# Kernel optimization log

Measured on AMD Instinct MI355X. Metric: run time of the kernel, lower is better.

## Reference

```python
import jax, jax.numpy as jnp
import numpy as np

EPS = 0.0  # GINConv eps

def _gin_conv(x, edge_index, W1, b1, W2, b2, n_nodes):
    # GINConv: mlp((1+eps)*x + sum_{j in N(i)} x_j)
    src, dst = edge_index[0], edge_index[1]
    agg = jax.ops.segment_sum(x[src], dst, num_segments=n_nodes)  # [N, d]
    h = (1.0 + EPS) * x + agg
    h = jax.nn.relu(h @ W1 + b1)  # Linear -> Identity(BN off) -> ReLU
    return h @ W2 + b2            # second Linear


def setup_inputs() -> dict:
    key = jax.random.key(0)
    ks = jax.random.split(key, 10)
    N, E = 50000, 600000
    d_in, d_hid, d_out = 128, 256, 128
    x = jax.random.normal(ks[0], (N, d_in), dtype=jnp.float32)
    edge_index = jax.random.randint(ks[1], (2, E), 0, N, dtype=jnp.int64)

    def lin(k, fan_in, fan_out):
        bound = 1.0 / np.sqrt(fan_in)
        kw, kb = jax.random.split(k)
        W = jax.random.uniform(kw, (fan_in, fan_out), jnp.float32, -bound, bound)
        b = jax.random.uniform(kb, (fan_out,), jnp.float32, -bound, bound)
        return W, b

    W1a, b1a = lin(ks[2], d_in, d_hid)   # conv0 mlp: 128->256
    W2a, b2a = lin(ks[3], d_hid, d_hid)  # conv0 mlp: 256->256
    W1b, b1b = lin(ks[4], d_hid, d_hid)  # conv1 mlp: 256->256
    W2b, b2b = lin(ks[5], d_hid, d_out)  # conv1 mlp: 256->128
    return {"x": x, "W1a": W1a, "b1a": b1a, "W2a": W2a, "b2a": b2a,
            "W1b": W1b, "b1b": b1b, "W2b": W2b, "b2b": b2b,
            "edge_index": edge_index}


def reference(x, W1a, b1a, W2a, b2a, W1b, b1b, W2b, b2b, edge_index):
    n_nodes = x.shape[0]
    # layer 0: GINConv -> relu (use_bn=False; dropout is identity in eval)
    h = _gin_conv(x, edge_index, W1a, b1a, W2a, b2a, n_nodes)
    h = jax.nn.relu(h)
    # final GINConv (no activation after, per forward())
    return _gin_conv(h, edge_index, W1b, b1b, W2b, b2b, n_nodes)
```

## Files before the change

### kernel.cpp

```cpp
#include <hip/hip_runtime.h>


typedef __bf16 bf16x8 __attribute__((ext_vector_type(8)));
typedef float f32x4 __attribute__((ext_vector_type(4)));
typedef float f32x2 __attribute__((ext_vector_type(2)));
typedef unsigned short u16x4 __attribute__((ext_vector_type(4)));
typedef unsigned short u16x8 __attribute__((ext_vector_type(8)));
typedef unsigned int uint32;
typedef uint32 u32x4 __attribute__((ext_vector_type(4)));

#define MAXDEG 48

__device__ __forceinline__ unsigned short f2bf(float f) {
  uint32 u = __builtin_bit_cast(uint32, f);
  u += 0x7FFFu + ((u >> 16) & 1u);
  return (unsigned short)(u >> 16);
}
__device__ __forceinline__ f32x2 bfpair(uint32 w) {
  f32x2 r;
  r.x = __builtin_bit_cast(float, w << 16);
  r.y = __builtin_bit_cast(float, w & 0xFFFF0000u);
  return r;
}

#define G2L16(gp, lp)                                                        \
  __builtin_amdgcn_global_load_lds(                                          \
      (const __attribute__((address_space(1))) void*)(gp),                   \
      (__attribute__((address_space(3))) void*)(lp), 16, 0, 0)

#define BARRIER()                                                            \
  do {                                                                       \
    asm volatile("" ::: "memory");                                           \
    __builtin_amdgcn_s_barrier();                                            \
    asm volatile("" ::: "memory");                                           \
  } while (0)
#define VMCNT0() asm volatile("s_waitcnt vmcnt(0)" ::: "memory")

__global__ __launch_bounds__(256) void prep_fill(
    const int* __restrict__ eidx, int* __restrict__ deg, int* __restrict__ ell,
    int E, int FB,
    const float* __restrict__ x, unsigned short* __restrict__ xb, long long n4,
    const float* __restrict__ W1a, const float* __restrict__ W2a,
    const float* __restrict__ W1b, const float* __restrict__ W2b,
    unsigned short* __restrict__ w1t, unsigned short* __restrict__ w2t,
    unsigned short* __restrict__ w3t, unsigned short* __restrict__ w4t) {
  int b = blockIdx.x;
  int t = threadIdx.x;
  if (b < FB) {
    int e = b * 256 + t;
    if (e < E) {
      int s = eidx[e];
      int d = eidx[e + E];
      int c = atomicAdd(&deg[d], 1);
      if (c < MAXDEG) ell[d * MAXDEG + c] = s;
    }
  } else if (b < FB + 768) {
    int i = (b - FB) * 256 + t;
    const float* W;
    unsigned short* WT;
    int K, N, j;
    if (i < 32768) {
      W = W1a; WT = w1t; K = 128; N = 256; j = i;
    } else if (i < 98304) {
      W = W2a; WT = w2t; K = 256; N = 256; j = i - 32768;
    } else if (i < 163840) {
      W = W1b; WT = w3t; K = 256; N = 256; j = i - 98304;
    } else {
      W = W2b; WT = w4t; K = 256; N = 128; j = i - 163840;
    }
    int k = j / N, n = j - k * N;
    WT[n * K + k] = f2bf(W[j]);
  } else {
    long long i = (long long)(b - FB - 768) * 256 + t;
    long long stride = (long long)(gridDim.x - FB - 768) * 256;
    for (; i < n4; i += stride) {
      float4 v = ((const float4*)x)[i];
      u16x4 o;
      o.x = f2bf(v.x); o.y = f2bf(v.y); o.z = f2bf(v.z); o.w = f2bf(v.w);
      ((u16x4*)xb)[i] = o;
    }
  }
}

template <int K1, int N2, bool OUT_BF16>
__global__ __launch_bounds__(512) void fused_layer(
    const unsigned short* __restrict__ src,
    const int* __restrict__ degv, const int* __restrict__ ell,
    const unsigned short* __restrict__ BT1, const float* __restrict__ b1,
    const unsigned short* __restrict__ BT2, const float* __restrict__ b2,
    void* __restrict__ Cout, int Nn) {
  constexpr int GRP = K1 / 8;
  __shared__ unsigned short Ash[64 * 264];
  __shared__ unsigned short Bs[2][256 * 32];
  const int tid = threadIdx.x;
  const int wave = tid >> 6, lane = tid & 63;
  const int quad = lane >> 4, l16 = lane & 15;
  const int rowBase = blockIdx.x * 64;

#define STAGE1B(buf, kk)                                                     \
  for (int c = tid; c < 1024; c += 512)                                      \
    G2L16(BT1 + (long long)(c >> 2) * K1 + (kk) + (c & 3) * 8,               \
          Bs[buf] + c * 8);
#define STAGE2B(buf, kk)                                                     \
  for (int c = tid; c < N2 * 4; c += 512)                                    \
    G2L16(BT2 + (long long)(c >> 2) * 256 + (kk) + (c & 3) * 8,              \
          Bs[buf] + c * 8);

  STAGE1B(0, 0);

  {
    constexpr int NPG = 64 * GRP / 512;
    const int gid = tid / GRP, gl = tid % GRP;
    const unsigned short* sp = src + gl * 8;
#pragma unroll
    for (int nn = 0; nn < NPG; ++nn) {
      const int lrow = gid * NPG + nn;
      int node = rowBase + lrow;
      if (node > Nn - 1) node = Nn - 1;
      const int beg = node * MAXDEG;
      int deg = degv[node];
      if (deg > MAXDEG) deg = MAXDEG;
      f32x2 acc[4];
      {
        u32x4 w = *(const u32x4*)(sp + (size_t)node * K1);
#pragma unroll
        for (int k = 0; k < 4; ++k) acc[k] = bfpair(w[k]);
      }
      int j = 0;
      for (; j + 8 <= deg; j += 8) {
        int idx[8];
#pragma unroll
        for (int u = 0; u < 8; ++u) idx[u] = ell[beg + j + u];
#pragma unroll
        for (int u = 0; u < 8; ++u) {
          u32x4 w = *(const u32x4*)(sp + (size_t)idx[u] * K1);
#pragma unroll
          for (int k = 0; k < 4; ++k) acc[k] += bfpair(w[k]);
        }
      }
      if (j < deg) {
#pragma unroll
        for (int u = 0; u < 8; ++u) {
          int jj = j + u;
          int e = beg + (jj < deg ? jj : deg - 1);
          float sel = (jj < deg) ? 1.f : 0.f;
          f32x2 fs = {sel, sel};
          int rv = ell[e];
          u32x4 w = *(const u32x4*)(sp + (size_t)rv * K1);
#pragma unroll
          for (int k = 0; k < 4; ++k) acc[k] += bfpair(w[k]) * fs;
        }
      }
      u16x8 o;
#pragma unroll
      for (int k = 0; k < 4; ++k) {
        o[2 * k] = f2bf(acc[k].x);
        o[2 * k + 1] = f2bf(acc[k].y);
      }
      *(u16x8*)(Ash + lrow * 264 + gl * 8) = o;
    }
  }
  __syncthreads();

  constexpr int nk1 = K1 / 32;
  f32x4 acc1[4][2] = {};
  int cur = 0;
  for (int t = 0; t < nk1; ++t) {
    if (t + 1 < nk1) STAGE1B(cur ^ 1, (t + 1) * 32);
    bf16x8 af[4], bfr[2];
#pragma unroll
    for (int mi = 0; mi < 4; ++mi)
      af[mi] = *(const bf16x8*)(Ash + (mi * 16 + l16) * 264 + t * 32 + quad * 8);
#pragma unroll
    for (int ni = 0; ni < 2; ++ni)
      bfr[ni] = *(const bf16x8*)(Bs[cur] + (wave * 32 + ni * 16 + l16) * 32 + quad * 8);
#pragma unroll
    for (int mi = 0; mi < 4; ++mi)
#pragma unroll
      for (int ni = 0; ni < 2; ++ni)
        acc1[mi][ni] = __builtin_amdgcn_mfma_f32_16x16x32_bf16(
            af[mi], bfr[ni], acc1[mi][ni], 0, 0, 0);
    VMCNT0();
    BARRIER();
    cur ^= 1;
  }

  STAGE2B(0, 0);
#pragma unroll
  for (int ni = 0; ni < 2; ++ni) {
    int col = wave * 32 + ni * 16 + l16;
    float bv = b1[col];
#pragma unroll
    for (int mi = 0; mi < 4; ++mi)
#pragma unroll
      for (int r = 0; r < 4; ++r) {
        int row = mi * 16 + quad * 4 + r;
        Ash[row * 264 + col] = f2bf(fmaxf(acc1[mi][ni][r] + bv, 0.f));
      }
  }
  __syncthreads();

  constexpr int NW2 = N2 / 8;
  constexpr int NI2 = NW2 / 16;
  f32x4 acc2[4][NI2] = {};
  cur = 0;
  for (int t = 0; t < 8; ++t) {
    int k2 = t * 32;
    if (t + 1 < 8) STAGE2B(cur ^ 1, k2 + 32);
    bf16x8 af[4], bfr[NI2];
#pragma unroll
    for (int mi = 0; mi < 4; ++mi)
      af[mi] = *(const bf16x8*)(Ash + (mi * 16 + l16) * 264 + k2 + quad * 8);
#pragma unroll
    for (int ni = 0; ni < NI2; ++ni)
      bfr[ni] = *(const bf16x8*)(Bs[cur] + (wave * NW2 + ni * 16 + l16) * 32 + quad * 8);
#pragma unroll
    for (int mi = 0; mi < 4; ++mi)
#pragma unroll
      for (int ni = 0; ni < NI2; ++ni)
        acc2[mi][ni] = __builtin_amdgcn_mfma_f32_16x16x32_bf16(
            af[mi], bfr[ni], acc2[mi][ni], 0, 0, 0);
    VMCNT0();
    BARRIER();
    cur ^= 1;
  }
#pragma unroll
  for (int ni = 0; ni < NI2; ++ni) {
    int col = wave * NW2 + ni * 16 + l16;
    float bv = b2[col];
#pragma unroll
    for (int mi = 0; mi < 4; ++mi)
#pragma unroll
      for (int r = 0; r < 4; ++r) {
        int row = rowBase + mi * 16 + quad * 4 + r;
        if (row < Nn) {
          float o = acc2[mi][ni][r] + bv;
          if (OUT_BF16)
            ((unsigned short*)Cout)[(long long)row * N2 + col] = f2bf(fmaxf(o, 0.f));
          else
            ((float*)Cout)[(long long)row * N2 + col] = o;
        }
      }
  }
#undef STAGE1B
#undef STAGE2B
}

extern "C" void kernel_launch(void* const* d_in, const int* in_sizes, int n_in,
                              void* d_out, int out_size, void* d_ws, size_t ws_size,
                              hipStream_t stream) {
  const float* x   = (const float*)d_in[0];
  const float* W1a = (const float*)d_in[1];
  const float* b1a = (const float*)d_in[2];
  const float* W2a = (const float*)d_in[3];
  const float* b2a = (const float*)d_in[4];
  const float* W1b = (const float*)d_in[5];
  const float* b1b = (const float*)d_in[6];
  const float* W2b = (const float*)d_in[7];
  const float* b2b = (const float*)d_in[8];
  const int*   ei  = (const int*)d_in[9];

  const int Nn = in_sizes[0] / 128;
  const int E  = in_sizes[9] / 2;
  float* out = (float*)d_out;

  unsigned short* h   = (unsigned short*)d_ws;
  unsigned short* xb  = h  + (size_t)Nn * 256;
  unsigned short* w1t = xb + (size_t)Nn * 128;
  unsigned short* w2t = w1t + 256 * 128;
  unsigned short* w3t = w2t + 256 * 256;
  unsigned short* w4t = w3t + 256 * 256;
  int* deg  = (int*)(w4t + 128 * 256);
  int* ell  = deg + Nn;

  dim3 blk(256);
  const int FB = (E + 255) / 256;

  hipMemsetAsync(deg, 0, (size_t)Nn * sizeof(int), stream);
  prep_fill<<<FB + 768 + 2048, blk, 0, stream>>>(
      ei, deg, ell, E, FB, x, xb, (long long)Nn * 128 / 4,
      W1a, W2a, W1b, W2b, w1t, w2t, w3t, w4t);

  int lb = (Nn + 63) / 64;

  fused_layer<128, 256, true><<<lb, dim3(512), 0, stream>>>(
      xb, deg, ell, w1t, b1a, w2t, b2a, h, Nn);
  fused_layer<256, 128, false><<<lb, dim3(512), 0, stream>>>(
      h, deg, ell, w3t, b1b, w4t, b2b, out, Nn);
}
```

Baseline: 250.7 us.

## Replace double-buffered weight staging with single LDS buffer and syncthreads

```diff
diff --git a/kernel.cpp b/kernel.cpp
--- a/kernel.cpp
+++ b/kernel.cpp
@@ -27,14 +27,6 @@
   __builtin_amdgcn_global_load_lds(                                          \
       (const __attribute__((address_space(1))) void*)(gp),                   \
       (__attribute__((address_space(3))) void*)(lp), 16, 0, 0)
-
-#define BARRIER()                                                            \
-  do {                                                                       \
-    asm volatile("" ::: "memory");                                           \
-    __builtin_amdgcn_s_barrier();                                            \
-    asm volatile("" ::: "memory");                                           \
-  } while (0)
-#define VMCNT0() asm volatile("s_waitcnt vmcnt(0)" ::: "memory")
 
 __global__ __launch_bounds__(256) void prep_fill(
     const int* __restrict__ eidx, int* __restrict__ deg, int* __restrict__ ell,
@@ -91,22 +83,20 @@
     void* __restrict__ Cout, int Nn) {
   constexpr int GRP = K1 / 8;
   __shared__ unsigned short Ash[64 * 264];
-  __shared__ unsigned short Bs[2][256 * 32];
+  __shared__ unsigned short Bs[256 * 32];
   const int tid = threadIdx.x;
   const int wave = tid >> 6, lane = tid & 63;
   const int quad = lane >> 4, l16 = lane & 15;
   const int rowBase = blockIdx.x * 64;
 
-#define STAGE1B(buf, kk)                                                     \
+#define STAGE1B(kk)                                                          \
   for (int c = tid; c < 1024; c += 512)                                      \
-    G2L16(BT1 + (long long)(c >> 2) * K1 + (kk) + (c & 3) * 8,               \
-          Bs[buf] + c * 8);
-#define STAGE2B(buf, kk)                                                     \
+    G2L16(BT1 + (long long)(c >> 2) * K1 + (kk) + (c & 3) * 8, Bs + c * 8);
+#define STAGE2B(kk)                                                          \
   for (int c = tid; c < N2 * 4; c += 512)                                    \
-    G2L16(BT2 + (long long)(c >> 2) * 256 + (kk) + (c & 3) * 8,              \
-          Bs[buf] + c * 8);
-
-  STAGE1B(0, 0);
+    G2L16(BT2 + (long long)(c >> 2) * 256 + (kk) + (c & 3) * 8, Bs + c * 8);
+
+  STAGE1B(0);
 
   {
     constexpr int NPG = 64 * GRP / 512;
@@ -164,28 +154,28 @@
 
   constexpr int nk1 = K1 / 32;
   f32x4 acc1[4][2] = {};
-  int cur = 0;
   for (int t = 0; t < nk1; ++t) {
-    if (t + 1 < nk1) STAGE1B(cur ^ 1, (t + 1) * 32);
+    if (t > 0) {
+      STAGE1B(t * 32);
+      __syncthreads();
+    }
     bf16x8 af[4], bfr[2];
 #pragma unroll
     for (int mi = 0; mi < 4; ++mi)
       af[mi] = *(const bf16x8*)(Ash + (mi * 16 + l16) * 264 + t * 32 + quad * 8);
 #pragma unroll
     for (int ni = 0; ni < 2; ++ni)
-      bfr[ni] = *(const bf16x8*)(Bs[cur] + (wave * 32 + ni * 16 + l16) * 32 + quad * 8);
+      bfr[ni] = *(const bf16x8*)(Bs + (wave * 32 + ni * 16 + l16) * 32 + quad * 8);
 #pragma unroll
     for (int mi = 0; mi < 4; ++mi)
 #pragma unroll
       for (int ni = 0; ni < 2; ++ni)
         acc1[mi][ni] = __builtin_amdgcn_mfma_f32_16x16x32_bf16(
             af[mi], bfr[ni], acc1[mi][ni], 0, 0, 0);
-    VMCNT0();
-    BARRIER();
-    cur ^= 1;
-  }
-
-  STAGE2B(0, 0);
+    __syncthreads();
+  }
+
+  STAGE2B(0);
 #pragma unroll
   for (int ni = 0; ni < 2; ++ni) {
     int col = wave * 32 + ni * 16 + l16;
@@ -203,26 +193,26 @@
   constexpr int NW2 = N2 / 8;
   constexpr int NI2 = NW2 / 16;
   f32x4 acc2[4][NI2] = {};
-  cur = 0;
   for (int t = 0; t < 8; ++t) {
+    if (t > 0) {
+      STAGE2B(t * 32);
+      __syncthreads();
+    }
     int k2 = t * 32;
-    if (t + 1 < 8) STAGE2B(cur ^ 1, k2 + 32);
     bf16x8 af[4], bfr[NI2];
 #pragma unroll
     for (int mi = 0; mi < 4; ++mi)
       af[mi] = *(const bf16x8*)(Ash + (mi * 16 + l16) * 264 + k2 + quad * 8);
 #pragma unroll
     for (int ni = 0; ni < NI2; ++ni)
-      bfr[ni] = *(const bf16x8*)(Bs[cur] + (wave * NW2 + ni * 16 + l16) * 32 + quad * 8);
+      bfr[ni] = *(const bf16x8*)(Bs + (wave * NW2 + ni * 16 + l16) * 32 + quad * 8);
 #pragma unroll
     for (int mi = 0; mi < 4; ++mi)
 #pragma unroll
       for (int ni = 0; ni < NI2; ++ni)
         acc2[mi][ni] = __builtin_amdgcn_mfma_f32_16x16x32_bf16(
             af[mi], bfr[ni], acc2[mi][ni], 0, 0, 0);
-    VMCNT0();
-    BARRIER();
-    cur ^= 1;
+    __syncthreads();
   }
 #pragma unroll
   for (int ni = 0; ni < NI2; ++ni) {
```

After: 253.9 us. No clear change (+1.3%).
